# Optimization experiments

Measured on AMD Instinct MI355X. Metric: run time of the kernel, lower is better.

Reference implementation:

```python
import jax, jax.numpy as jnp
import numpy as np

EMBED_DIM = 256
NUM_HEADS = 8


def positional_encoding(max_seq_len, embed_dim):
    # Faithful to torch source: exponent uses 2*i/embed_dim with raw column index i;
    # row 0 is all zeros; sin on even cols, cos on odd cols for rows 1:.
    pos = jnp.arange(max_seq_len, dtype=jnp.float32)[:, None]          # [L,1]
    i = jnp.arange(embed_dim, dtype=jnp.float32)[None, :]              # [1,D]
    angles = pos / jnp.power(10000.0, 2.0 * i / embed_dim)             # [L,D]
    pe = jnp.where((jnp.arange(embed_dim) % 2 == 0)[None, :],
                   jnp.sin(angles), jnp.cos(angles))
    pe = pe.at[0].set(0.0)
    return pe


def setup_inputs() -> dict:
    key = jax.random.key(0)
    ks = jax.random.split(key, 9)
    b, c, h, w = 4, EMBED_DIM, 48, 48
    d = EMBED_DIM  # internal_dim (downsample_rate=1)
    s = 1.0 / np.sqrt(d)
    inp = {
        "x": jax.random.normal(ks[0], (b, c, h, w), dtype=jnp.float32),
        "wq": jax.random.uniform(ks[1], (d, d), jnp.float32, -s, s),
        "bq": jax.random.uniform(ks[2], (d,), jnp.float32, -s, s),
        "wk": jax.random.uniform(ks[3], (d, d), jnp.float32, -s, s),
        "bk": jax.random.uniform(ks[4], (d,), jnp.float32, -s, s),
        "wv": jax.random.uniform(ks[5], (d, d), jnp.float32, -s, s),
        "bv": jax.random.uniform(ks[6], (d,), jnp.float32, -s, s),
        "wo": jax.random.uniform(ks[7], (d, d), jnp.float32, -s, s),
        "bo": jax.random.uniform(ks[8], (d,), jnp.float32, -s, s),
    }
    return inp


def reference(x, wq, bq, wk, bk, wv, bv, wo, bo):
    b, c, h, w = x.shape
    n = h * w
    H = NUM_HEADS
    dh = c // H
    xs = x.reshape(b, c, n).transpose(0, 2, 1)            # [b, n, c]
    xs = xs + positional_encoding(n, c)[None]             # add PE
    q = xs @ wq.T + bq                                    # [b, n, c]
    k = xs @ wk.T + bk
    v = xs @ wv.T + bv
    # separate heads -> [b, H, n, dh]
    q = q.reshape(b, n, H, dh).transpose(0, 2, 1, 3)
    k = k.reshape(b, n, H, dh).transpose(0, 2, 1, 3)
    v = v.reshape(b, n, H, dh).transpose(0, 2, 1, 3)
    attn = jnp.einsum("bhqd,bhkd->bhqk", q, k) / jnp.sqrt(jnp.float32(dh))
    attn = jax.nn.softmax(attn, axis=-1)
    out = jnp.einsum("bhqk,bhkd->bhqd", attn, v)          # [b, H, n, dh]
    out = out.transpose(0, 2, 1, 3).reshape(b, n, c)      # recombine heads
    out = out @ wo.T + bo                                 # out_proj
    return out.transpose(0, 2, 1).reshape(b, c, h, w)
```

## Files before the change

kernel.cpp:

```cpp
#include <hip/hip_runtime.h>

#define EMBED 256
#define NPOS  2304
#define BATCH 4
#define NH    8
#define DH    32

typedef float f32x4  __attribute__((ext_vector_type(4)));
typedef short bf16x8 __attribute__((ext_vector_type(8)));
typedef short s16x4  __attribute__((ext_vector_type(4)));
typedef unsigned u32x4 __attribute__((ext_vector_type(4)));

static __device__ __forceinline__ short f2b(float f) {
    union { float f; unsigned u; } c; c.f = f;
    unsigned r = (c.u + 0x7FFFu + ((c.u >> 16) & 1u)) >> 16;
    return (short)r;
}

static __device__ __forceinline__ unsigned cvtpk(float lo, float hi) {
    unsigned r;
    asm("v_cvt_pk_bf16_f32 %0, %1, %2" : "=v"(r) : "v"(lo), "v"(hi));
    return r;
}

static __device__ __forceinline__ float fexp2(float x) {
    float r;
    asm("v_exp_f32 %0, %1" : "=v"(r) : "v"(x));
    return r;
}

static __device__ __forceinline__ void plswap32(unsigned& a, unsigned& b) {
    asm("v_permlane32_swap_b32 %0, %1" : "+v"(a), "+v"(b));
}
static __device__ __forceinline__ void plswap16(unsigned& a, unsigned& b) {
    asm("v_permlane16_swap_b32 %0, %1" : "+v"(a), "+v"(b));
}

static __device__ __forceinline__ void gl_lds16(const short* g, short* l) {
    __builtin_amdgcn_global_load_lds(
        (const __attribute__((address_space(1))) unsigned int*)(g),
        (__attribute__((address_space(3))) unsigned int*)(l),
        16, 0, 0);
}

__global__ __launch_bounds__(256) void prep_all(
        const float* __restrict__ x,
        const float* __restrict__ wq, const float* __restrict__ wk,
        const float* __restrict__ wv, const float* __restrict__ wo,
        short* __restrict__ wqkv, short* __restrict__ wob,
        short* __restrict__ xs) {
    __shared__ float xt[32][65];
    int blk = blockIdx.x;
    int t = threadIdx.x;
    if (blk < 256) {
        int g4 = (blk * 256 + t) * 4;
        if (g4 < 196608) {
            int j = g4 >> 8, kk = g4 & 255;
            int proj = j >> 8, jj = j & 255;
            const float* s = (proj == 0) ? wq : (proj == 1) ? wk : wv;
            f32x4 w = *(const f32x4*)&s[jj * 256 + kk];
            s16x4 o4;
#pragma unroll
            for (int r = 0; r < 4; ++r) o4[r] = f2b(w[r]);
            *(s16x4*)&wqkv[g4] = o4;
        } else {
            int h2 = g4 - 196608;
            f32x4 w = *(const f32x4*)&wo[h2];
            s16x4 o4;
#pragma unroll
            for (int r = 0; r < 4; ++r) o4[r] = f2b(w[r]);
            *(s16x4*)&wob[h2] = o4;
        }
        return;
    }
    int bx = blk - 256;
    int b = bx / 288, rem = bx % 288;
    int c0 = (rem / 36) * 32, pos0 = (rem % 36) * 64;
    int j = t & 63, i0 = t >> 6;
    const float* xp = x + (size_t)(b * EMBED + c0) * NPOS + pos0;
#pragma unroll
    for (int rr = 0; rr < 8; ++rr) {
        int i = rr * 4 + i0;
        xt[i][j] = xp[(size_t)i * NPOS + j];
    }
    __syncthreads();
    int ii = (t & 15) * 2, jj0 = t >> 4;
    const float kln = -0.07195578415606394f;
#pragma unroll
    for (int pp = 0; pp < 4; ++pp) {
        int jj = pp * 16 + jj0;
        int pos = pos0 + jj;
        float v0 = xt[ii][jj], v1 = xt[ii + 1][jj];
        float pe0 = 0.f, pe1 = 0.f;
        if (pos > 0) {
            int c = c0 + ii;
            float a0 = (float)pos * __expf((float)c * kln);
            float a1 = (float)pos * __expf((float)(c + 1) * kln);
            pe0 = __sinf(a0);
            pe1 = __cosf(a1);
        }
        unsigned lo = (unsigned short)f2b(v0 + pe0);
        unsigned hi = (unsigned short)f2b(v1 + pe1);
        *reinterpret_cast<unsigned*>(xs + (size_t)(b * NPOS + pos) * EMBED + c0 + ii) =
            lo | (hi << 16);
    }
}

__global__ __launch_bounds__(256) void gemm_qkv(
        const short* __restrict__ A, const short* __restrict__ Bw,
        const float* __restrict__ bq, const float* __restrict__ bk,
        const float* __restrict__ bv,
        short* __restrict__ qd, short* __restrict__ kd, short* __restrict__ vtd) {
    __shared__ short a_sm[64 * 64];
    __shared__ short b_sm[64 * 64];
    int bx = blockIdx.x;
    int bm = bx / 12, bn = bx % 12;
    int m0 = bm * 64, n0 = bn * 64;
    int proj = bn >> 2;
    int t = threadIdx.x;
    int lane = t & 63, wid = t >> 6;
    int wm = wid >> 1, wn = wid & 1;
    int l15 = lane & 15, l4 = lane >> 4;

    int srow = t >> 2, sblk = t & 3;
    const short* ag = &A[(size_t)(m0 + srow) * 256 + sblk * 8];
    const short* bg = &Bw[(size_t)(n0 + srow) * 256 + sblk * 8];
    int sw0 = ((sblk ^ (srow & 7)) * 8);
    int sw1 = (((sblk + 4) ^ (srow & 7)) * 8);
    short* al0 = &a_sm[srow * 64 + sw0];
    short* al1 = &a_sm[srow * 64 + sw1];
    short* bl0 = &b_sm[srow * 64 + sw0];
    short* bl1 = &b_sm[srow * 64 + sw1];

    const float qs = 0.2550348623f;
    int b = bm / 36;
    int pos0 = m0 - b * NPOS;

    if (proj < 2) {
        const float* bias = (proj == 0) ? bq : bk;
        f32x4 acc[2][2];
#pragma unroll
        for (int mi = 0; mi < 2; ++mi) {
            int jj0 = (n0 & 255) + wm * 32 + mi * 16 + l4 * 4;
            f32x4 bi = {bias[jj0], bias[jj0 + 1], bias[jj0 + 2], bias[jj0 + 3]};
            acc[mi][0] = bi;
            acc[mi][1] = bi;
        }
        for (int ks = 0; ks < 4; ++ks) {
            __syncthreads();
            *(bf16x8*)al0 = *(const bf16x8*)(ag + ks * 64);
            *(bf16x8*)al1 = *(const bf16x8*)(ag + ks * 64 + 32);
            *(bf16x8*)bl0 = *(const bf16x8*)(bg + ks * 64);
            *(bf16x8*)bl1 = *(const bf16x8*)(bg + ks * 64 + 32);
            __syncthreads();
#pragma unroll
            for (int kk = 0; kk < 2; ++kk) {
                int blk = kk * 4 + l4;
                bf16x8 af[2], bf[2];
#pragma unroll
                for (int mi = 0; mi < 2; ++mi) {
                    int wr = wm * 32 + mi * 16 + l15;
                    af[mi] = *(const bf16x8*)&b_sm[wr * 64 + ((blk ^ (wr & 7)) * 8)];
                }
#pragma unroll
                for (int ni = 0; ni < 2; ++ni) {
                    int pr = wn * 32 + ni * 16 + l15;
                    bf[ni] = *(const bf16x8*)&a_sm[pr * 64 + ((blk ^ (pr & 7)) * 8)];
                }
#pragma unroll
                for (int mi = 0; mi < 2; ++mi)
#pragma unroll
                    for (int ni = 0; ni < 2; ++ni)
                        acc[mi][ni] = __builtin_amdgcn_mfma_f32_16x16x32_bf16(
                            af[mi], bf[ni], acc[mi][ni], 0, 0, 0);
            }
        }
        short* dst = (proj == 0) ? qd : kd;
        float sc = (proj == 0) ? qs : 1.0f;
#pragma unroll
        for (int mi = 0; mi < 2; ++mi) {
            int jj0 = (n0 & 255) + wm * 32 + mi * 16 + l4 * 4;
            int h = jj0 >> 5, d0 = jj0 & 31;
#pragma unroll
            for (int ni = 0; ni < 2; ++ni) {
                int pos = pos0 + wn * 32 + ni * 16 + l15;
                s16x4 pk;
#pragma unroll
                for (int r = 0; r < 4; ++r) pk[r] = f2b(acc[mi][ni][r] * sc);
                *(s16x4*)&dst[((size_t)(b * NH + h) * NPOS + pos) * DH + d0] = pk;
            }
        }
    } else {
        f32x4 acc[2][2];
#pragma unroll
        for (int ni = 0; ni < 2; ++ni) {
            int jj = (n0 & 255) + wn * 32 + ni * 16 + l15;
            float bias = bv[jj];
            f32x4 bi = {bias, bias, bias, bias};
            acc[0][ni] = bi;
            acc[1][ni] = bi;
        }
        for (int ks = 0; ks < 4; ++ks) {
            __syncthreads();
            *(bf16x8*)al0 = *(const bf16x8*)(ag + ks * 64);
            *(bf16x8*)al1 = *(const bf16x8*)(ag + ks * 64 + 32);
            *(bf16x8*)bl0 = *(const bf16x8*)(bg + ks * 64);
            *(bf16x8*)bl1 = *(const bf16x8*)(bg + ks * 64 + 32);
            __syncthreads();
#pragma unroll
            for (int kk = 0; kk < 2; ++kk) {
                int blk = kk * 4 + l4;
                bf16x8 af[2], bf[2];
#pragma unroll
                for (int mi = 0; mi < 2; ++mi) {
                    int ar = wm * 32 + mi * 16 + l15;
                    af[mi] = *(const bf16x8*)&a_sm[ar * 64 + ((blk ^ (ar & 7)) * 8)];
                }
#pragma unroll
                for (int ni = 0; ni < 2; ++ni) {
                    int br = wn * 32 + ni * 16 + l15;
                    bf[ni] = *(const bf16x8*)&b_sm[br * 64 + ((blk ^ (br & 7)) * 8)];
                }
#pragma unroll
                for (int mi = 0; mi < 2; ++mi)
#pragma unroll
                    for (int ni = 0; ni < 2; ++ni)
                        acc[mi][ni] = __builtin_amdgcn_mfma_f32_16x16x32_bf16(
                            af[mi], bf[ni], acc[mi][ni], 0, 0, 0);
            }
        }
#pragma unroll
        for (int mi = 0; mi < 2; ++mi) {
            int pos = pos0 + wm * 32 + mi * 16 + l4 * 4;
#pragma unroll
            for (int ni = 0; ni < 2; ++ni) {
                int jj = (n0 & 255) + wn * 32 + ni * 16 + l15;
                int h = jj >> 5, d = jj & 31;
                s16x4 pk;
#pragma unroll
                for (int r = 0; r < 4; ++r) pk[r] = f2b(acc[mi][ni][r]);
                *(s16x4*)&vtd[(((size_t)(b * NH + h) * 72 + (pos >> 5)) << 10)
                              + d * 32 + (pos & 31)] = pk;
            }
        }
    }
}


__global__ __launch_bounds__(256) void attn_fwd(
        const short* __restrict__ Q, const short* __restrict__ K,
        const short* __restrict__ VT, short* __restrict__ AO) {
    __shared__ short smem[16384];

    int bx0 = blockIdx.x;
    int bx = (bx0 & 7) * 144 + (bx0 >> 3);
    int bh = bx / 36, qg = bx % 36;
    int q0 = qg * 64;
    int t = threadIdx.x, lane = t & 63, wid = t >> 6;
    int l15 = lane & 15, l4 = lane >> 4;

    const short* Qb = Q + ((size_t)bh * NPOS + q0) * DH;
    bf16x8 qf[4];
#pragma unroll
    for (int qt = 0; qt < 4; ++qt)
        qf[qt] = *(const bf16x8*)&Qb[(qt * 16 + l15) * DH + l4 * 8];

    int kv0 = wid * 576;
    int ra = lane >> 2, blk = lane & 3;
    int swzk = (ra >> 1) & 3;
    int swzv = (ra & 3) ^ ((ra >> 2) & 3);
    const short* kga = K + ((size_t)bh * NPOS + kv0 + ra) * DH + ((blk ^ swzk) * 8);
    const short* vga = VT + (((size_t)bh * 72 + wid * 18) << 10)
                          + ra * 32 + ((blk ^ swzv) * 8);

    short* kbuf = smem + wid * 4096;
    short* vbuf = kbuf + 2048;

#pragma unroll
    for (int p = 0; p < 2; ++p) {
        gl_lds16(kga + p * 1024,            kbuf + p * 1024);
        gl_lds16(kga + p * 1024 + 16 * DH,  kbuf + p * 1024 + 512);
        gl_lds16(vga + p * 1024,            vbuf + p * 1024);
        gl_lds16(vga + p * 1024 + 512,      vbuf + p * 1024 + 512);
    }

    f32x4 zero = {0.f, 0.f, 0.f, 0.f};
    f32x4 o[2][4];
    f32x4 lacc[4];
#pragma unroll
    for (int qt = 0; qt < 4; ++qt) { o[0][qt] = zero; o[1][qt] = zero; lacc[qt] = zero; }
    const float MB = -17.312340490667561f;
    const f32x4 mb = {MB, MB, MB, MB};
    const u32x4 ones_u = {0x3F803F80u, 0x3F803F80u, 0x3F803F80u, 0x3F803F80u};
    const bf16x8 ones = __builtin_bit_cast(bf16x8, ones_u);

    int kswr = (l4 ^ ((l15 >> 1) & 3)) * 8;
    int vswr = (l4 ^ ((l15 & 3) ^ ((l15 >> 2) & 3))) * 8;

#pragma unroll 1
    for (int tt = 0; tt < 18; ++tt) {
        int buf = tt & 1;
        if (tt < 17) asm volatile("s_waitcnt vmcnt(4)" ::: "memory");
        else         asm volatile("s_waitcnt vmcnt(0)" ::: "memory");

        const short* kb = kbuf + buf * 1024;
        const short* vb = vbuf + buf * 1024;
        bf16x8 kf0 = *(const bf16x8*)&kb[l15 * 32 + kswr];
        bf16x8 kf1 = *(const bf16x8*)&kb[(16 + l15) * 32 + kswr];
        bf16x8 vf0 = *(const bf16x8*)&vb[l15 * 32 + vswr];
        bf16x8 vf1 = *(const bf16x8*)&vb[(16 + l15) * 32 + vswr];
        asm volatile("s_waitcnt lgkmcnt(0)" ::: "memory");
        __builtin_amdgcn_sched_barrier(0);

        if (tt + 2 < 18) {
            gl_lds16(kga + (tt + 2) * 1024,            kbuf + buf * 1024);
            gl_lds16(kga + (tt + 2) * 1024 + 16 * DH,  kbuf + buf * 1024 + 512);
            gl_lds16(vga + (tt + 2) * 1024,            vbuf + buf * 1024);
            gl_lds16(vga + (tt + 2) * 1024 + 512,      vbuf + buf * 1024 + 512);
        }

        __builtin_amdgcn_s_setprio(1);
#pragma unroll
        for (int qt = 0; qt < 4; ++qt) {
            f32x4 s0 = __builtin_amdgcn_mfma_f32_16x16x32_bf16(kf0, qf[qt], mb, 0, 0, 0);
            f32x4 s1 = __builtin_amdgcn_mfma_f32_16x16x32_bf16(kf1, qf[qt], mb, 0, 0, 0);

            float e00 = fexp2(s0[0]), e01 = fexp2(s0[1]), e02 = fexp2(s0[2]), e03 = fexp2(s0[3]);
            float e10 = fexp2(s1[0]), e11 = fexp2(s1[1]), e12 = fexp2(s1[2]), e13 = fexp2(s1[3]);

            unsigned p00 = cvtpk(e00, e01), p01 = cvtpk(e02, e03);
            unsigned p10 = cvtpk(e10, e11), p11 = cvtpk(e12, e13);
            unsigned a0 = p00, b0 = p10;
            plswap32(a0, b0); plswap16(a0, b0);
            unsigned a1 = p01, b1 = p11;
            plswap32(a1, b1); plswap16(a1, b1);
            u32x4 fr = {a0, a1, b0, b1};
            bf16x8 pf = __builtin_bit_cast(bf16x8, fr);

            o[0][qt] = __builtin_amdgcn_mfma_f32_16x16x32_bf16(vf0, pf, o[0][qt], 0, 0, 0);
            o[1][qt] = __builtin_amdgcn_mfma_f32_16x16x32_bf16(vf1, pf, o[1][qt], 0, 0, 0);
            lacc[qt] = __builtin_amdgcn_mfma_f32_16x16x32_bf16(ones, pf, lacc[qt], 0, 0, 0);
        }
        __builtin_amdgcn_s_setprio(0);
    }


    __syncthreads();
    if (wid > 0) {
        f32x4* od = (f32x4*)(smem + wid * 4096);
#pragma unroll
        for (int qt = 0; qt < 4; ++qt) {
#pragma unroll
            for (int dt = 0; dt < 2; ++dt)
                od[(qt * 2 + dt) * 64 + lane] = o[dt][qt];
        }
        if (l4 == 0) {
            float* ld = (float*)smem;
#pragma unroll
            for (int qt = 0; qt < 4; ++qt)
                ld[(wid - 1) * 64 + qt * 16 + l15] = lacc[qt][0];
        }
    }
    __syncthreads();
    if (wid == 0) {
        int b = bh >> 3, h = bh & 7;
        const float* ld = (const float*)smem;
#pragma unroll
        for (int qt = 0; qt < 4; ++qt) {
            float lt = lacc[qt][0] + ld[qt * 16 + l15] + ld[64 + qt * 16 + l15]
                     + ld[128 + qt * 16 + l15];
            float inv = __builtin_amdgcn_rcpf(lt);
            int qrow = q0 + qt * 16 + l15;
            size_t obase = ((size_t)b * NPOS + qrow) * EMBED + h * DH;
#pragma unroll
            for (int dt = 0; dt < 2; ++dt) {
                f32x4 ot = o[dt][qt];
#pragma unroll
                for (int w = 1; w < 4; ++w)
                    ot += ((const f32x4*)(smem + w * 4096))[(qt * 2 + dt) * 64 + lane];
                unsigned x0 = cvtpk(ot[0] * inv, ot[1] * inv);
                unsigned x1 = cvtpk(ot[2] * inv, ot[3] * inv);
                *(unsigned long long*)&AO[obase + dt * 16 + l4 * 4] =
                    (unsigned long long)x0 | ((unsigned long long)x1 << 32);
            }
        }
    }
}

__global__ __launch_bounds__(256) void gemm_out(
        const short* __restrict__ A, const short* __restrict__ Bw,
        const float* __restrict__ bo, float* __restrict__ out) {
    __shared__ short a_sm[32 * 64];
    __shared__ short b_sm[64 * 64];
    int bx = blockIdx.x;
    int bm = bx >> 2, bn = bx & 3;
    int m0 = bm * 32, n0 = bn * 64;
    int t = threadIdx.x;
    int lane = t & 63, wid = t >> 6;
    int wm = wid >> 1, wn = wid & 1;
    int l15 = lane & 15, l4 = lane >> 4;

    f32x4 acc[2];
#pragma unroll
    for (int ni = 0; ni < 2; ++ni) {
        float bias = bo[n0 + wn * 32 + ni * 16 + l15];
        f32x4 bi = {bias, bias, bias, bias};
        acc[ni] = bi;
    }

    int srow = t >> 2, sblk = t & 3;
    const short* ag = &A[(size_t)(m0 + srow) * 256 + sblk * 8];
    const short* bg = &Bw[(size_t)(n0 + srow) * 256 + sblk * 8];
    int sw0 = ((sblk ^ (srow & 7)) * 8);
    int sw1 = (((sblk + 4) ^ (srow & 7)) * 8);
    short* al0 = &a_sm[srow * 64 + sw0];
    short* al1 = &a_sm[srow * 64 + sw1];
    short* bl0 = &b_sm[srow * 64 + sw0];
    short* bl1 = &b_sm[srow * 64 + sw1];

    for (int ks = 0; ks < 4; ++ks) {
        __syncthreads();
        if (t < 128) {
            *(bf16x8*)al0 = *(const bf16x8*)(ag + ks * 64);
            *(bf16x8*)al1 = *(const bf16x8*)(ag + ks * 64 + 32);
        }
        *(bf16x8*)bl0 = *(const bf16x8*)(bg + ks * 64);
        *(bf16x8*)bl1 = *(const bf16x8*)(bg + ks * 64 + 32);
        __syncthreads();
#pragma unroll
        for (int kk = 0; kk < 2; ++kk) {
            int blk = kk * 4 + l4;
            int ar = wm * 16 + l15;
            bf16x8 af = *(const bf16x8*)&a_sm[ar * 64 + ((blk ^ (ar & 7)) * 8)];
            bf16x8 bf[2];
#pragma unroll
            for (int ni = 0; ni < 2; ++ni) {
                int br = wn * 32 + ni * 16 + l15;
                bf[ni] = *(const bf16x8*)&b_sm[br * 64 + ((blk ^ (br & 7)) * 8)];
            }
#pragma unroll
            for (int ni = 0; ni < 2; ++ni)
                acc[ni] = __builtin_amdgcn_mfma_f32_16x16x32_bf16(af, bf[ni], acc[ni], 0, 0, 0);
        }
    }

    int rowb = m0 + wm * 16 + l4 * 4;
    int b = rowb / NPOS;
    int pos = rowb - b * NPOS;
#pragma unroll
    for (int ni = 0; ni < 2; ++ni) {
        int jcol = n0 + wn * 32 + ni * 16 + l15;
        *(f32x4*)&out[((size_t)(b * EMBED) + jcol) * NPOS + pos] = acc[ni];
    }
}

extern "C" void kernel_launch(void* const* d_in, const int* in_sizes, int n_in,
                              void* d_out, int out_size, void* d_ws, size_t ws_size,
                              hipStream_t stream) {
    const float* x  = (const float*)d_in[0];
    const float* wq = (const float*)d_in[1];
    const float* bq = (const float*)d_in[2];
    const float* wk = (const float*)d_in[3];
    const float* bk = (const float*)d_in[4];
    const float* wv = (const float*)d_in[5];
    const float* bv = (const float*)d_in[6];
    const float* wo = (const float*)d_in[7];
    const float* bo = (const float*)d_in[8];

    char* ws = (char*)d_ws;
    short* wqkv = (short*)(ws);
    short* wob  = (short*)(ws + 393216);
    short* xs   = (short*)(ws + 524288);
    short* qb   = (short*)(ws + 5242880);
    short* kb   = (short*)(ws + 9961472);
    short* vtb  = (short*)(ws + 14680064);
    short* ao   = (short*)(ws + 19398656);
    float* out  = (float*)d_out;

    hipLaunchKernelGGL(prep_all, dim3(1408), dim3(256), 0, stream,
                       x, wq, wk, wv, wo, wqkv, wob, xs);
    hipLaunchKernelGGL(gemm_qkv, dim3(1728), dim3(256), 0, stream,
                       xs, wqkv, bq, bk, bv, qb, kb, vtb);
    hipLaunchKernelGGL(attn_fwd, dim3(1152), dim3(256), 0, stream, qb, kb, vtb, ao);
    hipLaunchKernelGGL(gemm_out, dim3(1152), dim3(256), 0, stream, ao, wob, bo, out);
}
```

Before: 67.75 us.

## Software-pipeline QK^T MFMAs one tile ahead of exp and PV in attention loop

```diff
diff --git a/kernel.cpp b/kernel.cpp
--- a/kernel.cpp
+++ b/kernel.cpp
@@ -265,10 +265,10 @@
     for (int qt = 0; qt < 4; ++qt)
         qf[qt] = *(const bf16x8*)&Qb[(qt * 16 + l15) * DH + l4 * 8];
 
-    int kv0 = wid * 576;
     int ra = lane >> 2, blk = lane & 3;
     int swzk = (ra >> 1) & 3;
     int swzv = (ra & 3) ^ ((ra >> 2) & 3);
+    int kv0 = wid * 576;
     const short* kga = K + ((size_t)bh * NPOS + kv0 + ra) * DH + ((blk ^ swzk) * 8);
     const short* vga = VT + (((size_t)bh * 72 + wid * 18) << 10)
                           + ra * 32 + ((blk ^ swzv) * 8);
@@ -297,8 +297,30 @@
     int kswr = (l4 ^ ((l15 >> 1) & 3)) * 8;
     int vswr = (l4 ^ ((l15 & 3) ^ ((l15 >> 2) & 3))) * 8;
 
+    f32x4 sP[4][2];
+    bf16x8 vfP0, vfP1;
+
+    {
+        asm volatile("s_waitcnt vmcnt(4)" ::: "memory");
+        bf16x8 kf0 = *(const bf16x8*)&kbuf[l15 * 32 + kswr];
+        bf16x8 kf1 = *(const bf16x8*)&kbuf[(16 + l15) * 32 + kswr];
+        vfP0 = *(const bf16x8*)&vbuf[l15 * 32 + vswr];
+        vfP1 = *(const bf16x8*)&vbuf[(16 + l15) * 32 + vswr];
+        asm volatile("s_waitcnt lgkmcnt(0)" ::: "memory");
+        __builtin_amdgcn_sched_barrier(0);
+        gl_lds16(kga + 2 * 1024,            kbuf);
+        gl_lds16(kga + 2 * 1024 + 16 * DH,  kbuf + 512);
+        gl_lds16(vga + 2 * 1024,            vbuf);
+        gl_lds16(vga + 2 * 1024 + 512,      vbuf + 512);
+#pragma unroll
+        for (int qt = 0; qt < 4; ++qt) {
+            sP[qt][0] = __builtin_amdgcn_mfma_f32_16x16x32_bf16(kf0, qf[qt], mb, 0, 0, 0);
+            sP[qt][1] = __builtin_amdgcn_mfma_f32_16x16x32_bf16(kf1, qf[qt], mb, 0, 0, 0);
+        }
+    }
+
 #pragma unroll 1
-    for (int tt = 0; tt < 18; ++tt) {
+    for (int tt = 1; tt < 18; ++tt) {
         int buf = tt & 1;
         if (tt < 17) asm volatile("s_waitcnt vmcnt(4)" ::: "memory");
         else         asm volatile("s_waitcnt vmcnt(0)" ::: "memory");
@@ -307,8 +329,8 @@
         const short* vb = vbuf + buf * 1024;
         bf16x8 kf0 = *(const bf16x8*)&kb[l15 * 32 + kswr];
         bf16x8 kf1 = *(const bf16x8*)&kb[(16 + l15) * 32 + kswr];
-        bf16x8 vf0 = *(const bf16x8*)&vb[l15 * 32 + vswr];
-        bf16x8 vf1 = *(const bf16x8*)&vb[(16 + l15) * 32 + vswr];
+        bf16x8 vN0 = *(const bf16x8*)&vb[l15 * 32 + vswr];
+        bf16x8 vN1 = *(const bf16x8*)&vb[(16 + l15) * 32 + vswr];
         asm volatile("s_waitcnt lgkmcnt(0)" ::: "memory");
         __builtin_amdgcn_sched_barrier(0);
 
@@ -320,13 +342,18 @@
         }
 
         __builtin_amdgcn_s_setprio(1);
+        f32x4 sN[4][2];
 #pragma unroll
         for (int qt = 0; qt < 4; ++qt) {
-            f32x4 s0 = __builtin_amdgcn_mfma_f32_16x16x32_bf16(kf0, qf[qt], mb, 0, 0, 0);
-            f32x4 s1 = __builtin_amdgcn_mfma_f32_16x16x32_bf16(kf1, qf[qt], mb, 0, 0, 0);
-
-            float e00 = fexp2(s0[0]), e01 = fexp2(s0[1]), e02 = fexp2(s0[2]), e03 = fexp2(s0[3]);
-            float e10 = fexp2(s1[0]), e11 = fexp2(s1[1]), e12 = fexp2(s1[2]), e13 = fexp2(s1[3]);
+            sN[qt][0] = __builtin_amdgcn_mfma_f32_16x16x32_bf16(kf0, qf[qt], mb, 0, 0, 0);
+            sN[qt][1] = __builtin_amdgcn_mfma_f32_16x16x32_bf16(kf1, qf[qt], mb, 0, 0, 0);
+        }
+#pragma unroll
+        for (int qt = 0; qt < 4; ++qt) {
+            float e00 = fexp2(sP[qt][0][0]), e01 = fexp2(sP[qt][0][1]);
+            float e02 = fexp2(sP[qt][0][2]), e03 = fexp2(sP[qt][0][3]);
+            float e10 = fexp2(sP[qt][1][0]), e11 = fexp2(sP[qt][1][1]);
+            float e12 = fexp2(sP[qt][1][2]), e13 = fexp2(sP[qt][1][3]);
 
             unsigned p00 = cvtpk(e00, e01), p01 = cvtpk(e02, e03);
             unsigned p10 = cvtpk(e10, e11), p11 = cvtpk(e12, e13);
@@ -337,8 +364,37 @@
             u32x4 fr = {a0, a1, b0, b1};
             bf16x8 pf = __builtin_bit_cast(bf16x8, fr);
 
-            o[0][qt] = __builtin_amdgcn_mfma_f32_16x16x32_bf16(vf0, pf, o[0][qt], 0, 0, 0);
-            o[1][qt] = __builtin_amdgcn_mfma_f32_16x16x32_bf16(vf1, pf, o[1][qt], 0, 0, 0);
+            o[0][qt] = __builtin_amdgcn_mfma_f32_16x16x32_bf16(vfP0, pf, o[0][qt], 0, 0, 0);
+            o[1][qt] = __builtin_amdgcn_mfma_f32_16x16x32_bf16(vfP1, pf, o[1][qt], 0, 0, 0);
+            lacc[qt] = __builtin_amdgcn_mfma_f32_16x16x32_bf16(ones, pf, lacc[qt], 0, 0, 0);
+        }
+        __builtin_amdgcn_s_setprio(0);
+#pragma unroll
+        for (int qt = 0; qt < 4; ++qt) { sP[qt][0] = sN[qt][0]; sP[qt][1] = sN[qt][1]; }
+        vfP0 = vN0;
+        vfP1 = vN1;
+    }
+
+    {
+        __builtin_amdgcn_s_setprio(1);
+#pragma unroll
+        for (int qt = 0; qt < 4; ++qt) {
+            float e00 = fexp2(sP[qt][0][0]), e01 = fexp2(sP[qt][0][1]);
+            float e02 = fexp2(sP[qt][0][2]), e03 = fexp2(sP[qt][0][3]);
+            float e10 = fexp2(sP[qt][1][0]), e11 = fexp2(sP[qt][1][1]);
+            float e12 = fexp2(sP[qt][1][2]), e13 = fexp2(sP[qt][1][3]);
+
+            unsigned p00 = cvtpk(e00, e01), p01 = cvtpk(e02, e03);
+            unsigned p10 = cvtpk(e10, e11), p11 = cvtpk(e12, e13);
+            unsigned a0 = p00, b0 = p10;
+            plswap32(a0, b0); plswap16(a0, b0);
+            unsigned a1 = p01, b1 = p11;
+            plswap32(a1, b1); plswap16(a1, b1);
+            u32x4 fr = {a0, a1, b0, b1};
+            bf16x8 pf = __builtin_bit_cast(bf16x8, fr);
+
+            o[0][qt] = __builtin_amdgcn_mfma_f32_16x16x32_bf16(vfP0, pf, o[0][qt], 0, 0, 0);
+            o[1][qt] = __builtin_amdgcn_mfma_f32_16x16x32_bf16(vfP1, pf, o[1][qt], 0, 0, 0);
             lacc[qt] = __builtin_amdgcn_mfma_f32_16x16x32_bf16(ones, pf, lacc[qt], 0, 0, 0);
         }
         __builtin_amdgcn_s_setprio(0);
```

New measurement: 73.75 us. 1.09x slower.
